# Optimization experiments

Hardware: AMD Instinct MI355X
Metric: run time of the kernel (lower is better)

The kernel has to match this reference:

```python
import jax, jax.numpy as jnp
import numpy as np

H = 180  # hidden size
T = 240  # timesteps

def lstm_cell_zero_state(x, Wih, bih, bhh):
    # torch nn.LSTMCell called with no (h, c): h = c = 0, so the W_hh term
    # vanishes and f-gate * c_prev vanishes. Gate order in torch: i, f, g, o.
    # x: [B, T, F] -> vectorized over all timesteps at once (no recurrence).
    gates = jnp.einsum('btf,gf->btg', x, Wih) + bih + bhh  # [B, T, 4H]
    i, f, g, o = jnp.split(gates, 4, axis=-1)
    c = jax.nn.sigmoid(i) * jnp.tanh(g)
    h = jax.nn.sigmoid(o) * jnp.tanh(c)
    return h  # [B, T, H]

def setup_inputs() -> dict:
    key = jax.random.key(0)
    ks = jax.random.split(key, 8)
    B = 2048
    s = lambda fan_in: 1.0 / np.sqrt(fan_in)
    x = jax.random.normal(ks[0], (B, 3, 60, T), dtype=jnp.float32)
    # Encoder LSTMCell(180 -> 180)
    W_ih_enc = jax.random.uniform(ks[1], (4 * H, 180), jnp.float32, -s(H), s(H))
    b_ih_enc = jax.random.uniform(ks[2], (4 * H,), jnp.float32, -s(H), s(H))
    b_hh_enc = jax.random.uniform(ks[3], (4 * H,), jnp.float32, -s(H), s(H))
    # Decoder LSTMCell(180 -> 180)
    W_ih_dec = jax.random.uniform(ks[4], (4 * H, H), jnp.float32, -s(H), s(H))
    b_ih_dec = jax.random.uniform(ks[5], (4 * H,), jnp.float32, -s(H), s(H))
    b_hh_dec = jax.random.uniform(ks[6], (4 * H,), jnp.float32, -s(H), s(H))
    # Output Linear(240*180 -> 40)
    W_out = jax.random.uniform(ks[7], (40, T * H), jnp.float32, -s(T * H), s(T * H))
    b_out = jnp.zeros((40,), jnp.float32)
    return {"x": x, "W_ih_enc": W_ih_enc, "b_ih_enc": b_ih_enc, "b_hh_enc": b_hh_enc,
            "W_ih_dec": W_ih_dec, "b_ih_dec": b_ih_dec, "b_hh_dec": b_hh_dec,
            "W_out": W_out, "b_out": b_out}

def reference(x, W_ih_enc, b_ih_enc, b_hh_enc, W_ih_dec, b_ih_dec, b_hh_dec, W_out, b_out):
    B = x.shape[0]
    # Encoder: [B,3,60,240] -> [B,240,3,60] -> [B,240,180]
    xe = jnp.transpose(x, (0, 3, 1, 2)).reshape(B, T, 3 * 60)
    h_enc = lstm_cell_zero_state(xe, W_ih_enc, b_ih_enc, b_hh_enc)  # [B,T,H]
    enc = jax.nn.softmax(h_enc, axis=2)
    # Decoder LSTM (also zero-state every step)
    h_dec = lstm_cell_zero_state(enc, W_ih_dec, b_ih_dec, b_hh_dec)  # [B,T,H]
    flat = h_dec.reshape(B, T * H)
    logits = flat @ W_out.T + b_out  # [B,40]
    out = jax.nn.softmax(logits.reshape(B, 4, 10), axis=2)
    return out
```

## Files before the change

kernel.cpp:

```cpp
#include <hip/hip_runtime.h>
#include <hip/hip_bf16.h>

#define HH 180
#define TT 240
#define KP 192
#define MP 576
#define LSTR 194
#define KOUT 43200
#define BB 2048

typedef __attribute__((ext_vector_type(8))) short short8;
typedef __attribute__((ext_vector_type(4))) float float4v;

__device__ inline unsigned short f2bf(float f) {
    unsigned u = __builtin_bit_cast(unsigned, f);
    u += 0x7fffu + ((u >> 16) & 1u);
    return (unsigned short)(u >> 16);
}
__device__ inline float bf2f(unsigned short h) {
    unsigned u = ((unsigned)h) << 16;
    return __builtin_bit_cast(float, u);
}
__device__ inline float sigm(float x) {
    return __builtin_amdgcn_rcpf(1.f + __expf(-x));
}
__device__ inline float tanh_(float x) {
    return 2.f * __builtin_amdgcn_rcpf(1.f + __expf(-2.f * x)) - 1.f;
}

__global__ void prep_kernel(const float* __restrict__ W1, const float* __restrict__ bi1,
                            const float* __restrict__ bh1, const float* __restrict__ W2,
                            const float* __restrict__ bi2, const float* __restrict__ bh2,
                            const float* __restrict__ Wo,
                            unsigned short* __restrict__ W1p, unsigned short* __restrict__ W2p,
                            float* __restrict__ bEp, float* __restrict__ bDp,
                            unsigned short* __restrict__ Wop, float* __restrict__ logits)
{
    int id = blockIdx.x * 256 + threadIdx.x;
    if (id < MP * KP) {
        int mp = id / KP, k = id % KP;
        int g = mp / KP, h = mp % KP;
        unsigned short v1 = 0, v2 = 0;
        if (h < HH && k < HH) {
            int r = (g == 0) ? h : (g == 1 ? 360 + h : 540 + h);
            v1 = f2bf(W1[r * HH + k]);
            v2 = f2bf(W2[r * HH + k]);
        }
        W1p[id] = v1; W2p[id] = v2;
    }
    if (id < MP) {
        int g = id / KP, h = id % KP;
        float v1 = 0.f, v2 = 0.f;
        if (h < HH) {
            int r = (g == 0) ? h : (g == 1 ? 360 + h : 540 + h);
            v1 = bi1[r] + bh1[r];
            v2 = bi2[r] + bh2[r];
        }
        bEp[id] = v1; bDp[id] = v2;
    }
    if (id < 48 * KOUT) {
        int n = id / KOUT, k = id % KOUT;
        Wop[id] = (n < 40) ? f2bf(Wo[n * KOUT + k]) : (unsigned short)0;
    }
    if (id < BB * 40) logits[id] = 0.f;
}

__global__ __launch_bounds__(256, 2) void phaseA_kernel(
    const float* __restrict__ x, const unsigned short* __restrict__ W1p,
    const unsigned short* __restrict__ W2p, const float* __restrict__ bEp,
    const float* __restrict__ bDp, unsigned short* __restrict__ hdec)
{
    __shared__ __align__(16) unsigned short Xs[128 * LSTR];
    __shared__ float bEs[MP], bDs[MP], sred[256];

    const int tid = threadIdx.x;
    const int b = blockIdx.x >> 1;
    const int t0 = (blockIdx.x & 1) * 112;
    const float* xb = x + (size_t)b * HH * TT;

    for (int i = tid; i < MP; i += 256) { bEs[i] = bEp[i]; bDs[i] = bDp[i]; }

    {
        const int c = tid & 127, half = tid >> 7;
        unsigned* lu = (unsigned*)Xs;
        const int cbase = c * (LSTR / 2);
        for (int i = 0; i < 45; ++i) {
            int f = half * 90 + 2 * i;
            float a0 = xb[f * TT + t0 + c];
            float a1 = xb[(f + 1) * TT + t0 + c];
            lu[cbase + (f >> 1)] = (unsigned)f2bf(a0) | ((unsigned)f2bf(a1) << 16);
        }
        if (half == 0) {
            for (int j = 0; j < 7; ++j) lu[cbase + 90 + j] = 0u;
        }
    }
    __syncthreads();

    const int lane = tid & 63, wv = tid >> 6;
    const int ch = wv >> 1, par = wv & 1;
    const int l15 = lane & 15, l4 = lane >> 4;

    short8 Bf[4][6];
    {
        const unsigned* lu = (const unsigned*)Xs;
        for (int nt = 0; nt < 4; ++nt) {
            int col = ch * 64 + nt * 16 + l15;
            int base = col * (LSTR / 2) + l4 * 4;
            #pragma unroll
            for (int ks = 0; ks < 6; ++ks) {
                union { unsigned u[4]; short8 v; } t;
                int idx = base + ks * 16;
                t.u[0] = lu[idx]; t.u[1] = lu[idx + 1];
                t.u[2] = lu[idx + 2]; t.u[3] = lu[idx + 3];
                Bf[nt][ks] = t.v;
            }
        }
    }
    __syncthreads();

    {
        const uint4* W1q = (const uint4*)W1p;
        for (int tri = par; tri < 12; tri += 2) {
            float4v acc[3][4];
            #pragma unroll
            for (int s = 0; s < 3; ++s)
                #pragma unroll
                for (int n = 0; n < 4; ++n) acc[s][n] = (float4v){0.f, 0.f, 0.f, 0.f};
            #pragma unroll
            for (int sec = 0; sec < 3; ++sec) {
                int abase = (sec * KP + tri * 16 + l15) * (KP / 8) + l4;
                #pragma unroll
                for (int ks = 0; ks < 6; ++ks) {
                    union { uint4 q; short8 v; } a;
                    a.q = W1q[abase + ks * 4];
                    #pragma unroll
                    for (int nt = 0; nt < 4; ++nt)
                        acc[sec][nt] = __builtin_amdgcn_mfma_f32_16x16x32_bf16(
                            a.v, Bf[nt][ks], acc[sec][nt], 0, 0, 0);
                }
            }
            unsigned* lw = (unsigned*)Xs;
            const int h0 = tri * 16 + l4 * 4;
            #pragma unroll
            for (int nt = 0; nt < 4; ++nt) {
                int col = ch * 64 + nt * 16 + l15;
                unsigned pk[2];
                #pragma unroll
                for (int e = 0; e < 4; ++e) {
                    int h = h0 + e;
                    float gi = acc[0][nt][e] + bEs[h];
                    float gg = acc[1][nt][e] + bEs[KP + h];
                    float go = acc[2][nt][e] + bEs[2 * KP + h];
                    float cc = sigm(gi) * tanh_(gg);
                    float hv = sigm(go) * tanh_(cc);
                    ((unsigned short*)pk)[e] = f2bf(__expf(hv));
                }
                lw[col * (LSTR / 2) + (h0 >> 1)] = pk[0];
                lw[col * (LSTR / 2) + (h0 >> 1) + 1] = pk[1];
            }
        }
    }
    __syncthreads();

    {
        const int c = tid & 127, half = tid >> 7;
        const unsigned* lu = (const unsigned*)Xs;
        int base = c * (LSTR / 2) + half * 45;
        float s = 0.f;
        for (int j = 0; j < 45; ++j) {
            unsigned u = lu[base + j];
            s += bf2f((unsigned short)u) + bf2f((unsigned short)(u >> 16));
        }
        sred[half * 128 + c] = s;
    }
    __syncthreads();

    {
        const unsigned* lu = (const unsigned*)Xs;
        for (int nt = 0; nt < 4; ++nt) {
            int col = ch * 64 + nt * 16 + l15;
            int base = col * (LSTR / 2) + l4 * 4;
            #pragma unroll
            for (int ks = 0; ks < 6; ++ks) {
                union { unsigned u[4]; short8 v; } t;
                int idx = base + ks * 16;
                t.u[0] = lu[idx]; t.u[1] = lu[idx + 1];
                t.u[2] = lu[idx + 2]; t.u[3] = lu[idx + 3];
                Bf[nt][ks] = t.v;
            }
        }
    }
    float rs[4];
    #pragma unroll
    for (int nt = 0; nt < 4; ++nt) {
        int col = ch * 64 + nt * 16 + l15;
        rs[nt] = __builtin_amdgcn_rcpf(sred[col] + sred[128 + col]);
    }

    {
        const uint4* W2q = (const uint4*)W2p;
        unsigned short* hout = hdec + (size_t)b * TT * HH;
        for (int tri = par; tri < 12; tri += 2) {
            float4v acc[3][4];
            #pragma unroll
            for (int s = 0; s < 3; ++s)
                #pragma unroll
                for (int n = 0; n < 4; ++n) acc[s][n] = (float4v){0.f, 0.f, 0.f, 0.f};
            #pragma unroll
            for (int sec = 0; sec < 3; ++sec) {
                int abase = (sec * KP + tri * 16 + l15) * (KP / 8) + l4;
                #pragma unroll
                for (int ks = 0; ks < 6; ++ks) {
                    union { uint4 q; short8 v; } a;
                    a.q = W2q[abase + ks * 4];
                    #pragma unroll
                    for (int nt = 0; nt < 4; ++nt)
                        acc[sec][nt] = __builtin_amdgcn_mfma_f32_16x16x32_bf16(
                            a.v, Bf[nt][ks], acc[sec][nt], 0, 0, 0);
                }
            }
            const int h0 = tri * 16 + l4 * 4;
            if (h0 < HH) {
                #pragma unroll
                for (int nt = 0; nt < 4; ++nt) {
                    int col = ch * 64 + nt * 16 + l15;
                    unsigned pk[2];
                    #pragma unroll
                    for (int e = 0; e < 4; ++e) {
                        int h = h0 + e;
                        float gi = acc[0][nt][e] * rs[nt] + bDs[h];
                        float gg = acc[1][nt][e] * rs[nt] + bDs[KP + h];
                        float go = acc[2][nt][e] * rs[nt] + bDs[2 * KP + h];
                        float cc = sigm(gi) * tanh_(gg);
                        float hv = sigm(go) * tanh_(cc);
                        ((unsigned short*)pk)[e] = f2bf(hv);
                    }
                    uint2 pv; pv.x = pk[0]; pv.y = pk[1];
                    *(uint2*)(hout + (size_t)(t0 + col) * HH + h0) = pv;
                }
            }
        }
    }
}

__global__ __launch_bounds__(256, 4) void phaseB_kernel(
    const unsigned short* __restrict__ hdec, const unsigned short* __restrict__ Wop,
    float* __restrict__ logits)
{
    const int tid = threadIdx.x;
    const int lane = tid & 63, wv = tid >> 6;
    const int l15 = lane & 15, l4 = lane >> 4;
    const int m0 = blockIdx.x * 64 + wv * 16;
    const int k0 = blockIdx.y * 1440;

    const uint4* Aq = (const uint4*)hdec;
    const uint4* Bq = (const uint4*)Wop;
    const int QK = KOUT / 8;
    int abase = (m0 + l15) * QK + (k0 >> 3) + l4;
    int bbase = l15 * QK + (k0 >> 3) + l4;

    float4v acc[3];
    #pragma unroll
    for (int n = 0; n < 3; ++n) acc[n] = (float4v){0.f, 0.f, 0.f, 0.f};

    #pragma unroll 3
    for (int ks = 0; ks < 45; ++ks) {
        union { uint4 q; short8 v; } a, b0, b1, b2;
        a.q  = Aq[abase + ks * 4];
        b0.q = Bq[bbase + ks * 4];
        b1.q = Bq[bbase + 16 * QK + ks * 4];
        b2.q = Bq[bbase + 32 * QK + ks * 4];
        acc[0] = __builtin_amdgcn_mfma_f32_16x16x32_bf16(a.v, b0.v, acc[0], 0, 0, 0);
        acc[1] = __builtin_amdgcn_mfma_f32_16x16x32_bf16(a.v, b1.v, acc[1], 0, 0, 0);
        acc[2] = __builtin_amdgcn_mfma_f32_16x16x32_bf16(a.v, b2.v, acc[2], 0, 0, 0);
    }

    #pragma unroll
    for (int nt = 0; nt < 3; ++nt) {
        int o = nt * 16 + l15;
        if (o < 40) {
            #pragma unroll
            for (int e = 0; e < 4; ++e) {
                int row = m0 + l4 * 4 + e;
                atomicAdd(&logits[row * 40 + o], acc[nt][e]);
            }
        }
    }
}

__global__ void out_kernel(const float* __restrict__ logits, const float* __restrict__ bout,
                           float* __restrict__ out)
{
    int id = blockIdx.x * 256 + threadIdx.x;
    if (id >= BB * 4) return;
    int b = id >> 2, j = id & 3;
    float v[10], mx = -1e30f;
    #pragma unroll
    for (int d = 0; d < 10; ++d) {
        v[d] = logits[b * 40 + j * 10 + d] + bout[j * 10 + d];
        mx = fmaxf(mx, v[d]);
    }
    float s = 0.f;
    #pragma unroll
    for (int d = 0; d < 10; ++d) { v[d] = __expf(v[d] - mx); s += v[d]; }
    float r = __builtin_amdgcn_rcpf(s);
    #pragma unroll
    for (int d = 0; d < 10; ++d) out[b * 40 + j * 10 + d] = v[d] * r;
}

extern "C" void kernel_launch(void* const* d_in, const int* in_sizes, int n_in,
                              void* d_out, int out_size, void* d_ws, size_t ws_size,
                              hipStream_t stream)
{
    const float* x    = (const float*)d_in[0];
    const float* W1   = (const float*)d_in[1];
    const float* bi1  = (const float*)d_in[2];
    const float* bh1  = (const float*)d_in[3];
    const float* W2   = (const float*)d_in[4];
    const float* bi2  = (const float*)d_in[5];
    const float* bh2  = (const float*)d_in[6];
    const float* Wo   = (const float*)d_in[7];
    const float* bout = (const float*)d_in[8];

    char* ws = (char*)d_ws;
    unsigned short* W1p = (unsigned short*)(ws + 0);
    unsigned short* W2p = (unsigned short*)(ws + 221184);
    float* bEp          = (float*)(ws + 442368);
    float* bDp          = (float*)(ws + 444928);
    unsigned short* Wop = (unsigned short*)(ws + 447488);
    float* logits       = (float*)(ws + 4594688);
    unsigned short* hdec= (unsigned short*)(ws + 4922368);

    prep_kernel<<<(48 * KOUT + 255) / 256, 256, 0, stream>>>(
        W1, bi1, bh1, W2, bi2, bh2, Wo, W1p, W2p, bEp, bDp, Wop, logits);
    phaseA_kernel<<<BB * 2, 256, 0, stream>>>(x, W1p, W2p, bEp, bDp, hdec);
    phaseB_kernel<<<dim3(32, 30), 256, 0, stream>>>(hdec, Wop, logits);
    out_kernel<<<(BB * 4 + 255) / 256, 256, 0, stream>>>(logits, bout, (float*)d_out);
}
```

Measured before the change: 1.058 ms.

## Split phaseA into 64-timestep tiles with fused softmax row-sum reduction

Each batch row is now split into four 64-timestep chunks instead of two 112/128 chunks. This halves shared memory and B-fragment registers so more blocks fit per CU, with launch bounds raised to 4. The softmax denominator is now accumulated in registers during the encoder epilogue and reduced with shuffles, which removes a separate LDS pass and one barrier. Bf16 packing uses the paired conversion intrinsic. The last chunk overlaps earlier timesteps (176..239), so some work is recomputed and the W1/W2 weights are fetched by twice as many blocks.

```diff
diff --git a/kernel.cpp b/kernel.cpp
--- a/kernel.cpp
+++ b/kernel.cpp
@@ -6,6 +6,7 @@
 #define KP 192
 #define MP 576
 #define LSTR 194
+#define LSTRD 97
 #define KOUT 43200
 #define BB 2048
 
@@ -17,9 +18,10 @@
     u += 0x7fffu + ((u >> 16) & 1u);
     return (unsigned short)(u >> 16);
 }
-__device__ inline float bf2f(unsigned short h) {
-    unsigned u = ((unsigned)h) << 16;
-    return __builtin_bit_cast(float, u);
+__device__ inline unsigned pack_bf2(float a, float b) {
+    union { __hip_bfloat162 h; unsigned u; } t;
+    t.h = __float22bfloat162_rn(make_float2(a, b));
+    return t.u;
 }
 __device__ inline float sigm(float x) {
     return __builtin_amdgcn_rcpf(1.f + __expf(-x));
@@ -65,33 +67,35 @@
     if (id < BB * 40) logits[id] = 0.f;
 }
 
-__global__ __launch_bounds__(256, 2) void phaseA_kernel(
+__global__ __launch_bounds__(256, 4) void phaseA_kernel(
     const float* __restrict__ x, const unsigned short* __restrict__ W1p,
     const unsigned short* __restrict__ W2p, const float* __restrict__ bEp,
     const float* __restrict__ bDp, unsigned short* __restrict__ hdec)
 {
-    __shared__ __align__(16) unsigned short Xs[128 * LSTR];
-    __shared__ float bEs[MP], bDs[MP], sred[256];
+    __shared__ __align__(16) unsigned short Xs[64 * LSTR];
+    __shared__ float bEs[MP], bDs[MP];
+    __shared__ float sred[2][64];
 
     const int tid = threadIdx.x;
-    const int b = blockIdx.x >> 1;
-    const int t0 = (blockIdx.x & 1) * 112;
+    const int b = blockIdx.x >> 2;
+    const int chunk = blockIdx.x & 3;
+    const int t0 = (chunk < 3) ? 64 * chunk : 176;
     const float* xb = x + (size_t)b * HH * TT;
 
     for (int i = tid; i < MP; i += 256) { bEs[i] = bEp[i]; bDs[i] = bDp[i]; }
 
     {
-        const int c = tid & 127, half = tid >> 7;
+        const int c = tid & 63, q = tid >> 6;
         unsigned* lu = (unsigned*)Xs;
-        const int cbase = c * (LSTR / 2);
-        for (int i = 0; i < 45; ++i) {
-            int f = half * 90 + 2 * i;
-            float a0 = xb[f * TT + t0 + c];
-            float a1 = xb[(f + 1) * TT + t0 + c];
-            lu[cbase + (f >> 1)] = (unsigned)f2bf(a0) | ((unsigned)f2bf(a1) << 16);
-        }
-        if (half == 0) {
-            for (int j = 0; j < 7; ++j) lu[cbase + 90 + j] = 0u;
+        const int cbase = c * LSTRD;
+        for (int p = q; p < 90; p += 4) {
+            float a0 = xb[(size_t)(2 * p) * TT + t0 + c];
+            float a1 = xb[(size_t)(2 * p + 1) * TT + t0 + c];
+            lu[cbase + p] = pack_bf2(a0, a1);
+        }
+        if (q == 3) {
+            #pragma unroll
+            for (int j = 90; j < LSTRD; ++j) lu[cbase + j] = 0u;
         }
     }
     __syncthreads();
@@ -100,12 +104,13 @@
     const int ch = wv >> 1, par = wv & 1;
     const int l15 = lane & 15, l4 = lane >> 4;
 
-    short8 Bf[4][6];
+    short8 Bf[2][6];
     {
         const unsigned* lu = (const unsigned*)Xs;
-        for (int nt = 0; nt < 4; ++nt) {
-            int col = ch * 64 + nt * 16 + l15;
-            int base = col * (LSTR / 2) + l4 * 4;
+        #pragma unroll
+        for (int nt = 0; nt < 2; ++nt) {
+            int col = ch * 32 + nt * 16 + l15;
+            int base = col * LSTRD + l4 * 4;
             #pragma unroll
             for (int ks = 0; ks < 6; ++ks) {
                 union { unsigned u[4]; short8 v; } t;
@@ -118,14 +123,16 @@
     }
     __syncthreads();
 
+    float esum[2] = {0.f, 0.f};
     {
         const uint4* W1q = (const uint4*)W1p;
         for (int tri = par; tri < 12; tri += 2) {
-            float4v acc[3][4];
-            #pragma unroll
-            for (int s = 0; s < 3; ++s)
-                #pragma unroll
-                for (int n = 0; n < 4; ++n) acc[s][n] = (float4v){0.f, 0.f, 0.f, 0.f};
+            float4v acc[3][2];
+            #pragma unroll
+            for (int s = 0; s < 3; ++s) {
+                acc[s][0] = (float4v){0.f, 0.f, 0.f, 0.f};
+                acc[s][1] = (float4v){0.f, 0.f, 0.f, 0.f};
+            }
             #pragma unroll
             for (int sec = 0; sec < 3; ++sec) {
                 int abase = (sec * KP + tri * 16 + l15) * (KP / 8) + l4;
@@ -133,18 +140,18 @@
                 for (int ks = 0; ks < 6; ++ks) {
                     union { uint4 q; short8 v; } a;
                     a.q = W1q[abase + ks * 4];
-                    #pragma unroll
-                    for (int nt = 0; nt < 4; ++nt)
-                        acc[sec][nt] = __builtin_amdgcn_mfma_f32_16x16x32_bf16(
-                            a.v, Bf[nt][ks], acc[sec][nt], 0, 0, 0);
+                    acc[sec][0] = __builtin_amdgcn_mfma_f32_16x16x32_bf16(
+                        a.v, Bf[0][ks], acc[sec][0], 0, 0, 0);
+                    acc[sec][1] = __builtin_amdgcn_mfma_f32_16x16x32_bf16(
+                        a.v, Bf[1][ks], acc[sec][1], 0, 0, 0);
                 }
             }
             unsigned* lw = (unsigned*)Xs;
             const int h0 = tri * 16 + l4 * 4;
             #pragma unroll
-            for (int nt = 0; nt < 4; ++nt) {
-                int col = ch * 64 + nt * 16 + l15;
-                unsigned pk[2];
+            for (int nt = 0; nt < 2; ++nt) {
+                int col = ch * 32 + nt * 16 + l15;
+                float ev[4];
                 #pragma unroll
                 for (int e = 0; e < 4; ++e) {
                     int h = h0 + e;
@@ -152,34 +159,39 @@
                     float gg = acc[1][nt][e] + bEs[KP + h];
                     float go = acc[2][nt][e] + bEs[2 * KP + h];
                     float cc = sigm(gi) * tanh_(gg);
-                    float hv = sigm(go) * tanh_(cc);
-                    ((unsigned short*)pk)[e] = f2bf(__expf(hv));
+                    ev[e] = __expf(sigm(go) * tanh_(cc));
                 }
-                lw[col * (LSTR / 2) + (h0 >> 1)] = pk[0];
-                lw[col * (LSTR / 2) + (h0 >> 1) + 1] = pk[1];
-            }
-        }
+                if (h0 + 4 <= HH)
+                    esum[nt] += (ev[0] + ev[1]) + (ev[2] + ev[3]);
+                lw[col * LSTRD + (h0 >> 1)]     = pack_bf2(ev[0], ev[1]);
+                lw[col * LSTRD + (h0 >> 1) + 1] = pack_bf2(ev[2], ev[3]);
+            }
+        }
+    }
+
+    esum[0] += __shfl_xor(esum[0], 16);
+    esum[0] += __shfl_xor(esum[0], 32);
+    esum[1] += __shfl_xor(esum[1], 16);
+    esum[1] += __shfl_xor(esum[1], 32);
+    if (lane < 16) {
+        sred[par][ch * 32 + l15]      = esum[0];
+        sred[par][ch * 32 + 16 + l15] = esum[1];
     }
     __syncthreads();
 
-    {
-        const int c = tid & 127, half = tid >> 7;
+    float rs[2];
+    #pragma unroll
+    for (int nt = 0; nt < 2; ++nt) {
+        int col = ch * 32 + nt * 16 + l15;
+        rs[nt] = __builtin_amdgcn_rcpf(sred[0][col] + sred[1][col]);
+    }
+
+    {
         const unsigned* lu = (const unsigned*)Xs;
-        int base = c * (LSTR / 2) + half * 45;
-        float s = 0.f;
-        for (int j = 0; j < 45; ++j) {
-            unsigned u = lu[base + j];
-            s += bf2f((unsigned short)u) + bf2f((unsigned short)(u >> 16));
-        }
-        sred[half * 128 + c] = s;
-    }
-    __syncthreads();
-
-    {
-        const unsigned* lu = (const unsigned*)Xs;
-        for (int nt = 0; nt < 4; ++nt) {
-            int col = ch * 64 + nt * 16 + l15;
-            int base = col * (LSTR / 2) + l4 * 4;
+        #pragma unroll
+        for (int nt = 0; nt < 2; ++nt) {
+            int col = ch * 32 + nt * 16 + l15;
+            int base = col * LSTRD + l4 * 4;
             #pragma unroll
             for (int ks = 0; ks < 6; ++ks) {
                 union { unsigned u[4]; short8 v; } t;
@@ -190,22 +202,17 @@
             }
         }
     }
-    float rs[4];
-    #pragma unroll
-    for (int nt = 0; nt < 4; ++nt) {
-        int col = ch * 64 + nt * 16 + l15;
-        rs[nt] = __builtin_amdgcn_rcpf(sred[col] + sred[128 + col]);
-    }
 
     {
         const uint4* W2q = (const uint4*)W2p;
         unsigned short* hout = hdec + (size_t)b * TT * HH;
         for (int tri = par; tri < 12; tri += 2) {
-            float4v acc[3][4];
-            #pragma unroll
-            for (int s = 0; s < 3; ++s)
-                #pragma unroll
-                for (int n = 0; n < 4; ++n) acc[s][n] = (float4v){0.f, 0.f, 0.f, 0.f};
+            float4v acc[3][2];
+            #pragma unroll
+            for (int s = 0; s < 3; ++s) {
+                acc[s][0] = (float4v){0.f, 0.f, 0.f, 0.f};
+                acc[s][1] = (float4v){0.f, 0.f, 0.f, 0.f};
+            }
             #pragma unroll
             for (int sec = 0; sec < 3; ++sec) {
                 int abase = (sec * KP + tri * 16 + l15) * (KP / 8) + l4;
@@ -213,18 +220,20 @@
                 for (int ks = 0; ks < 6; ++ks) {
                     union { uint4 q; short8 v; } a;
                     a.q = W2q[abase + ks * 4];
-                    #pragma unroll
-                    for (int nt = 0; nt < 4; ++nt)
-                        acc[sec][nt] = __builtin_amdgcn_mfma_f32_16x16x32_bf16(
-                            a.v, Bf[nt][ks], acc[sec][nt], 0, 0, 0);
+                    acc[sec][0] = __builtin_amdgcn_mfma_f32_16x16x32_bf16(
+                        a.v, Bf[0][ks], acc[sec][0], 0, 0, 0);
+                    acc[sec][1] = __builtin_amdgcn_mfma_f32_16x16x32_bf16(
+                        a.v, Bf[1][ks], acc[sec][1], 0, 0, 0);
                 }
             }
             const int h0 = tri * 16 + l4 * 4;
             if (h0 < HH) {
                 #pragma unroll
-                for (int nt = 0; nt < 4; ++nt) {
-                    int col = ch * 64 + nt * 16 + l15;
+                for (int nt = 0; nt < 2; ++nt) {
+                    int col = ch * 32 + nt * 16 + l15;
+                    float gi0, gg0, go0;
                     unsigned pk[2];
+                    float o[4];
                     #pragma unroll
                     for (int e = 0; e < 4; ++e) {
                         int h = h0 + e;
@@ -232,9 +241,10 @@
                         float gg = acc[1][nt][e] * rs[nt] + bDs[KP + h];
                         float go = acc[2][nt][e] * rs[nt] + bDs[2 * KP + h];
                         float cc = sigm(gi) * tanh_(gg);
-                        float hv = sigm(go) * tanh_(cc);
-                        ((unsigned short*)pk)[e] = f2bf(hv);
+                        o[e] = sigm(go) * tanh_(cc);
                     }
+                    pk[0] = pack_bf2(o[0], o[1]);
+                    pk[1] = pack_bf2(o[2], o[3]);
                     uint2 pv; pv.x = pk[0]; pv.y = pk[1];
                     *(uint2*)(hout + (size_t)(t0 + col) * HH + h0) = pv;
                 }
@@ -333,7 +343,7 @@
 
     prep_kernel<<<(48 * KOUT + 255) / 256, 256, 0, stream>>>(
         W1, bi1, bh1, W2, bi2, bh2, Wo, W1p, W2p, bEp, bDp, Wop, logits);
-    phaseA_kernel<<<BB * 2, 256, 0, stream>>>(x, W1p, W2p, bEp, bDp, hdec);
+    phaseA_kernel<<<BB * 4, 256, 0, stream>>>(x, W1p, W2p, bEp, bDp, hdec);
     phaseB_kernel<<<dim3(32, 30), 256, 0, stream>>>(hdec, Wop, logits);
     out_kernel<<<(BB * 4 + 255) / 256, 256, 0, stream>>>(logits, bout, (float*)d_out);
 }
```

Result: slower. 1.306 ms (+23.5%).
